# Optimization experiments

Measured on AMD Instinct MI355X. Metric: run time of the kernel, lower is better.

## Reference

```python
import jax, jax.numpy as jnp
import numpy as np


def _sparsify24(w):
    """2:4 structured sparsity: per contiguous group of 4 along the last dim,
    keep the 2 largest-magnitude entries, zero the other 2 (soft_threshold24)."""
    m, n = w.shape
    g = w.reshape(m, n // 4, 4)
    a = jnp.abs(g)
    # 2nd-largest magnitude in each group = index 2 of ascending sort of 4
    thresh = jnp.sort(a, axis=-1)[..., 2:3]
    mask = a >= thresh
    return (g * mask).reshape(m, n)


def setup_inputs() -> dict:
    key = jax.random.key(0)
    k1, k2, k3 = jax.random.split(key, 3)
    B, S, DIN, DOUT = 4, 4096, 1024, 1024
    x = jax.random.normal(k1, (B, S, DIN), dtype=jnp.float32)
    weight = jax.random.normal(k2, (DIN, DOUT), dtype=jnp.float32) * 0.02
    bias = jax.random.normal(k3, (DOUT,), dtype=jnp.float32) * 0.02
    sparse_scale = jnp.ones((1,), dtype=jnp.float32)
    return {"x": x, "weight": weight, "bias": bias, "sparse_scale": sparse_scale}


def reference(x, weight, bias, sparse_scale):
    # get_sparse_weight: cast weight to fp16, apply 2:4 sparsity, multiply by
    # learnable fp32 scale (promotes to fp32 as in torch half*float).
    w_sparse = _sparsify24(weight.astype(jnp.float16)).astype(jnp.float32) * sparse_scale
    # fake_fp8_mm: both operands cast to fp16, accumulate/output in fp32.
    a = x.reshape(-1, x.shape[-1]).astype(jnp.float16)          # [B*S, DIN]
    b = w_sparse.astype(jnp.float16)                             # [DIN, DOUT]
    out = jnp.matmul(a, b, preferred_element_type=jnp.float32)   # [B*S, DOUT] fp32
    out = out.reshape(*x.shape[:-1], -1) + bias
    return out
```

## Files before the change

### kernel.cpp

```cpp
#include <hip/hip_runtime.h>
#include <hip/hip_fp16.h>
#include <stdint.h>

#define M_TOT 16384
#define N_TOT 1024
#define K_TOT 1024

typedef _Float16 f16x8 __attribute__((ext_vector_type(8)));
typedef float f32x4 __attribute__((ext_vector_type(4)));
typedef unsigned short ushort4v __attribute__((ext_vector_type(4)));

__device__ inline void gl2lds16(const void* g, void* l) {
    __builtin_amdgcn_global_load_lds(
        (const __attribute__((address_space(1))) void*)(uintptr_t)(g),
        (__attribute__((address_space(3))) void*)(uint32_t)(uintptr_t)(l),
        16, 0, 0);
}

__global__ void __launch_bounds__(256) prep_and_cast(const float* __restrict__ X,
                                                     const float* __restrict__ W,
                                                     const float* __restrict__ scale_p,
                                                     _Float16* __restrict__ Xh,
                                                     _Float16* __restrict__ wT) {
    const int tid = threadIdx.x;
    if (blockIdx.x < 256) {
        __shared__ _Float16 sT[64 * 68 + 4];
        const float scale = scale_p[0];
        const int k0 = (blockIdx.x & 15) * 64;
        const int n0 = (blockIdx.x >> 4) * 64;
        const int r = tid >> 4;
        const int c4 = (tid & 15) * 4;
#pragma unroll
        for (int p = 0; p < 4; ++p) {
            const int k = p * 16 + r;
            float4 w4 = *(const float4*)&W[(size_t)(k0 + k) * N_TOT + n0 + c4];
            _Float16 h0 = (_Float16)w4.x, h1 = (_Float16)w4.y, h2 = (_Float16)w4.z, h3 = (_Float16)w4.w;
            float a0 = fabsf((float)h0), a1 = fabsf((float)h1), a2 = fabsf((float)h2), a3 = fabsf((float)h3);
            float lo01 = fminf(a0, a1), hi01 = fmaxf(a0, a1);
            float lo23 = fminf(a2, a3), hi23 = fmaxf(a2, a3);
            float s2 = fmaxf(fminf(hi01, hi23), fmaxf(lo01, lo23));
            sT[(c4 + 0) * 68 + k] = (_Float16)(((a0 >= s2) ? (float)h0 : 0.0f) * scale);
            sT[(c4 + 1) * 68 + k] = (_Float16)(((a1 >= s2) ? (float)h1 : 0.0f) * scale);
            sT[(c4 + 2) * 68 + k] = (_Float16)(((a2 >= s2) ? (float)h2 : 0.0f) * scale);
            sT[(c4 + 3) * 68 + k] = (_Float16)(((a3 >= s2) ? (float)h3 : 0.0f) * scale);
        }
        __syncthreads();
#pragma unroll
        for (int p = 0; p < 4; ++p) {
            const int n = p * 16 + r;
            ushort4v v = *(const ushort4v*)&sT[n * 68 + c4];
            *(ushort4v*)&wT[(size_t)(n0 + n) * K_TOT + k0 + c4] = v;
        }
    } else {
        size_t i = ((size_t)(blockIdx.x - 256) * 256 + tid) * 8;
        float4 x0 = *(const float4*)&X[i];
        float4 x1 = *(const float4*)&X[i + 4];
        f16x8 h;
        h[0] = (_Float16)x0.x; h[1] = (_Float16)x0.y; h[2] = (_Float16)x0.z; h[3] = (_Float16)x0.w;
        h[4] = (_Float16)x1.x; h[5] = (_Float16)x1.y; h[6] = (_Float16)x1.z; h[7] = (_Float16)x1.w;
        *(f16x8*)&Xh[i] = h;
    }
}

__global__ void __launch_bounds__(512, 2) gemm_bt(const _Float16* __restrict__ A,
                                                  const _Float16* __restrict__ Bt,
                                                  const float* __restrict__ bias,
                                                  float* __restrict__ C) {
    __shared__ __align__(16) _Float16 sA[2][2][256 * 32];
    __shared__ __align__(16) _Float16 sB[2][2][256 * 32];

    const int tid = threadIdx.x;
    const int id = blockIdx.x;
    const int by = id & 63;
    const int bx = id >> 6;
    const int wave = tid >> 6;
    const int lane = tid & 63;
    const int wm = wave >> 2;
    const int wn = wave & 3;
    const int quad = lane >> 4;
    const int l16 = lane & 15;

    const int row0 = tid >> 2;
    const int s4 = tid & 3;
    const int g = s4 ^ ((row0 >> 1) & 3);
    const _Float16* gA = A + (size_t)(by * 256 + row0) * K_TOT + g * 8;
    const _Float16* gB = Bt + (size_t)(bx * 256 + row0) * K_TOT + g * 8;
    const int dst0 = row0 * 32 + s4 * 8;

    const int rdoff = l16 * 64 + ((quad ^ ((l16 >> 1) & 3)) << 4);

    f32x4 acc[8][4];
#pragma unroll
    for (int i = 0; i < 8; ++i)
#pragma unroll
        for (int j = 0; j < 4; ++j)
            acc[i][j] = (f32x4){0.f, 0.f, 0.f, 0.f};
    f16x8 fa[4], fb[4];

#define STAGE_A(b, kt, kh) do {                                            \
        const _Float16* s_ = gA + (kt) * 64 + (kh) * 32;                   \
        gl2lds16(s_, &sA[b][kh][dst0]);                                    \
        gl2lds16(s_ + (size_t)128 * K_TOT, &sA[b][kh][dst0 + 128 * 32]);   \
    } while (0)
#define STAGE_B(b, kt, kh) do {                                            \
        const _Float16* s_ = gB + (kt) * 64 + (kh) * 32;                   \
        gl2lds16(s_, &sB[b][kh][dst0]);                                    \
        gl2lds16(s_ + (size_t)128 * K_TOT, &sB[b][kh][dst0 + 128 * 32]);   \
    } while (0)
#define FENCE asm volatile("" ::: "memory")
#define WAIT8 asm volatile("s_waitcnt vmcnt(8)" ::: "memory")
#define BAR do { FENCE; __builtin_amdgcn_s_barrier(); FENCE; } while (0)

#define PHASE(b, ks, qm, LOADB, STAGE_STMT) do {                                   \
        {                                                                          \
            const char* bA_ = (const char*)&sA[b][ks][0] + rdoff + wm * 8192 + (qm) * 4096; \
            fa[0] = *(const f16x8*)(bA_);                                          \
            fa[1] = *(const f16x8*)(bA_ + 1024);                                   \
            fa[2] = *(const f16x8*)(bA_ + 2048);                                   \
            fa[3] = *(const f16x8*)(bA_ + 3072);                                   \
            if (LOADB) {                                                           \
                const char* bB_ = (const char*)&sB[b][ks][0] + rdoff + wn * 4096;  \
                fb[0] = *(const f16x8*)(bB_);                                      \
                fb[1] = *(const f16x8*)(bB_ + 1024);                               \
                fb[2] = *(const f16x8*)(bB_ + 2048);                               \
                fb[3] = *(const f16x8*)(bB_ + 3072);                               \
            }                                                                      \
        }                                                                          \
        STAGE_STMT;                                                                \
        BAR;                                                                       \
        __builtin_amdgcn_s_setprio(1);                                             \
        _Pragma("unroll")                                                          \
        for (int ii = 0; ii < 4; ++ii) {                                           \
            _Pragma("unroll")                                                      \
            for (int j = 0; j < 4; ++j)                                            \
                acc[(qm) * 4 + ii][j] = __builtin_amdgcn_mfma_f32_16x16x32_f16(    \
                    fa[ii], fb[j], acc[(qm) * 4 + ii][j], 0, 0, 0);                \
        }                                                                          \
        __builtin_amdgcn_s_setprio(0);                                             \
    } while (0)

    STAGE_A(0, 0, 0); STAGE_B(0, 0, 0);
    STAGE_A(0, 0, 1); STAGE_B(0, 0, 1);
    STAGE_A(1, 1, 0); STAGE_B(1, 1, 0);
    WAIT8;
    BAR;

    for (int it = 0; it < 8; ++it) {
        const int t1 = (2 * it + 1) & 15;
        const int t2 = (2 * it + 2) & 15;
        const int t3 = (2 * it + 3) & 15;
        PHASE(0, 0, 0, 1, STAGE_A(1, t1, 1));        BAR;
        PHASE(0, 0, 1, 0, STAGE_B(1, t1, 1)); WAIT8; BAR;
        PHASE(0, 1, 0, 1, STAGE_A(0, t2, 0));        BAR;
        PHASE(0, 1, 1, 0, STAGE_B(0, t2, 0)); WAIT8; BAR;
        PHASE(1, 0, 0, 1, STAGE_A(0, t2, 1));        BAR;
        PHASE(1, 0, 1, 0, STAGE_B(0, t2, 1)); WAIT8; BAR;
        PHASE(1, 1, 0, 1, STAGE_A(1, t3, 0));        BAR;
        PHASE(1, 1, 1, 0, STAGE_B(1, t3, 0)); WAIT8; BAR;
    }

#pragma unroll
    for (int j = 0; j < 4; ++j) {
        const int col = bx * 256 + wn * 64 + j * 16 + l16;
        const float bj = bias[col];
#pragma unroll
        for (int mi = 0; mi < 8; ++mi) {
            const int row0o = by * 256 + wm * 128 + mi * 16 + quad * 4;
#pragma unroll
            for (int r = 0; r < 4; ++r) {
                C[(size_t)(row0o + r) * N_TOT + col] = acc[mi][j][r] + bj;
            }
        }
    }

#undef PHASE
#undef BAR
#undef WAIT8
#undef FENCE
#undef STAGE_B
#undef STAGE_A
}

extern "C" void kernel_launch(void* const* d_in, const int* in_sizes, int n_in,
                              void* d_out, int out_size, void* d_ws, size_t ws_size,
                              hipStream_t stream) {
    const float* x      = (const float*)d_in[0];
    const float* weight = (const float*)d_in[1];
    const float* bias   = (const float*)d_in[2];
    const float* sscale = (const float*)d_in[3];
    float* out = (float*)d_out;

    _Float16* wT = (_Float16*)d_ws;
    _Float16* xh = (_Float16*)((char*)d_ws + (size_t)2 * 1024 * 1024);

    prep_and_cast<<<256 + (M_TOT * K_TOT / 8) / 256, 256, 0, stream>>>(x, weight, sscale, xh, wT);
    gemm_bt<<<256, 512, 0, stream>>>(xh, wT, bias, out);
}
```

Measured before the change: 152.6 us.

## Replace double-buffered half-tile pipeline with triple-buffered single-barrier K loop

Restructures the GEMM main loop from a double-buffered scheme to a three-stage ring of 32-wide K tiles. Each tile stages A and B together, and each phase needs one wait-and-barrier instead of two barriers. Each phase now loads all eight A fragments and four B fragments and issues 32 MFMAs, which cuts synchronisation overhead and gives loads more lead time. The cost is more vector registers for fragments and a three-buffer LDS footprint, along with waitcnt accounting that depends on an exact count of outstanding loads.

Measured after the change: 152.0 us. No clear change (-0.4%).

```diff
diff --git a/kernel.cpp b/kernel.cpp
--- a/kernel.cpp
+++ b/kernel.cpp
@@ -66,8 +66,8 @@
                                                   const _Float16* __restrict__ Bt,
                                                   const float* __restrict__ bias,
                                                   float* __restrict__ C) {
-    __shared__ __align__(16) _Float16 sA[2][2][256 * 32];
-    __shared__ __align__(16) _Float16 sB[2][2][256 * 32];
+    __shared__ __align__(16) _Float16 sA[3][256 * 32];
+    __shared__ __align__(16) _Float16 sB[3][256 * 32];
 
     const int tid = threadIdx.x;
     const int id = blockIdx.x;
@@ -95,69 +95,55 @@
 #pragma unroll
         for (int j = 0; j < 4; ++j)
             acc[i][j] = (f32x4){0.f, 0.f, 0.f, 0.f};
-    f16x8 fa[4], fb[4];
+    f16x8 fa[8], fb[4];
 
-#define STAGE_A(b, kt, kh) do {                                            \
-        const _Float16* s_ = gA + (kt) * 64 + (kh) * 32;                   \
-        gl2lds16(s_, &sA[b][kh][dst0]);                                    \
-        gl2lds16(s_ + (size_t)128 * K_TOT, &sA[b][kh][dst0 + 128 * 32]);   \
-    } while (0)
-#define STAGE_B(b, kt, kh) do {                                            \
-        const _Float16* s_ = gB + (kt) * 64 + (kh) * 32;                   \
-        gl2lds16(s_, &sB[b][kh][dst0]);                                    \
-        gl2lds16(s_ + (size_t)128 * K_TOT, &sB[b][kh][dst0 + 128 * 32]);   \
+#define STAGE(t, b) do {                                                   \
+        const _Float16* sa_ = gA + (size_t)(t) * 32;                       \
+        gl2lds16(sa_, &sA[b][dst0]);                                       \
+        gl2lds16(sa_ + (size_t)128 * K_TOT, &sA[b][dst0 + 128 * 32]);      \
+        const _Float16* sb_ = gB + (size_t)(t) * 32;                       \
+        gl2lds16(sb_, &sB[b][dst0]);                                       \
+        gl2lds16(sb_ + (size_t)128 * K_TOT, &sB[b][dst0 + 128 * 32]);      \
     } while (0)
 #define FENCE asm volatile("" ::: "memory")
-#define WAIT8 asm volatile("s_waitcnt vmcnt(8)" ::: "memory")
-#define BAR do { FENCE; __builtin_amdgcn_s_barrier(); FENCE; } while (0)
 
-#define PHASE(b, ks, qm, LOADB, STAGE_STMT) do {                                   \
+#define PH(b, t2, b2, DO_STAGE, WLAST) do {                                        \
+        if (WLAST) asm volatile("s_waitcnt vmcnt(0)" ::: "memory");                \
+        else       asm volatile("s_waitcnt vmcnt(4)" ::: "memory");                \
+        __builtin_amdgcn_sched_barrier(0);                                         \
+        __builtin_amdgcn_s_barrier();                                              \
+        FENCE;                                                                     \
+        if (DO_STAGE) STAGE(t2, b2);                                               \
         {                                                                          \
-            const char* bA_ = (const char*)&sA[b][ks][0] + rdoff + wm * 8192 + (qm) * 4096; \
-            fa[0] = *(const f16x8*)(bA_);                                          \
-            fa[1] = *(const f16x8*)(bA_ + 1024);                                   \
-            fa[2] = *(const f16x8*)(bA_ + 2048);                                   \
-            fa[3] = *(const f16x8*)(bA_ + 3072);                                   \
-            if (LOADB) {                                                           \
-                const char* bB_ = (const char*)&sB[b][ks][0] + rdoff + wn * 4096;  \
-                fb[0] = *(const f16x8*)(bB_);                                      \
-                fb[1] = *(const f16x8*)(bB_ + 1024);                               \
-                fb[2] = *(const f16x8*)(bB_ + 2048);                               \
-                fb[3] = *(const f16x8*)(bB_ + 3072);                               \
-            }                                                                      \
+            const char* bA_ = (const char*)&sA[b][0] + rdoff + wm * 8192;          \
+            const char* bB_ = (const char*)&sB[b][0] + rdoff + wn * 4096;          \
+            _Pragma("unroll")                                                      \
+            for (int j = 0; j < 4; ++j) fb[j] = *(const f16x8*)(bB_ + j * 1024);   \
+            _Pragma("unroll")                                                      \
+            for (int i = 0; i < 8; ++i) fa[i] = *(const f16x8*)(bA_ + i * 1024);   \
         }                                                                          \
-        STAGE_STMT;                                                                \
-        BAR;                                                                       \
         __builtin_amdgcn_s_setprio(1);                                             \
         _Pragma("unroll")                                                          \
-        for (int ii = 0; ii < 4; ++ii) {                                           \
+        for (int i = 0; i < 8; ++i) {                                              \
             _Pragma("unroll")                                                      \
             for (int j = 0; j < 4; ++j)                                            \
-                acc[(qm) * 4 + ii][j] = __builtin_amdgcn_mfma_f32_16x16x32_f16(    \
-                    fa[ii], fb[j], acc[(qm) * 4 + ii][j], 0, 0, 0);                \
+                acc[i][j] = __builtin_amdgcn_mfma_f32_16x16x32_f16(                \
+                    fa[i], fb[j], acc[i][j], 0, 0, 0);                             \
         }                                                                          \
         __builtin_amdgcn_s_setprio(0);                                             \
     } while (0)
 
-    STAGE_A(0, 0, 0); STAGE_B(0, 0, 0);
-    STAGE_A(0, 0, 1); STAGE_B(0, 0, 1);
-    STAGE_A(1, 1, 0); STAGE_B(1, 1, 0);
-    WAIT8;
-    BAR;
+    STAGE(0, 0);
+    STAGE(1, 1);
 
-    for (int it = 0; it < 8; ++it) {
-        const int t1 = (2 * it + 1) & 15;
-        const int t2 = (2 * it + 2) & 15;
-        const int t3 = (2 * it + 3) & 15;
-        PHASE(0, 0, 0, 1, STAGE_A(1, t1, 1));        BAR;
-        PHASE(0, 0, 1, 0, STAGE_B(1, t1, 1)); WAIT8; BAR;
-        PHASE(0, 1, 0, 1, STAGE_A(0, t2, 0));        BAR;
-        PHASE(0, 1, 1, 0, STAGE_B(0, t2, 0)); WAIT8; BAR;
-        PHASE(1, 0, 0, 1, STAGE_A(0, t2, 1));        BAR;
-        PHASE(1, 0, 1, 0, STAGE_B(0, t2, 1)); WAIT8; BAR;
-        PHASE(1, 1, 0, 1, STAGE_A(1, t3, 0));        BAR;
-        PHASE(1, 1, 1, 0, STAGE_B(1, t3, 0)); WAIT8; BAR;
+    for (int it = 0; it < 10; ++it) {
+        const int t = 3 * it;
+        PH(0, t + 2, 2, 1, 0);
+        PH(1, t + 3, 0, 1, 0);
+        PH(2, t + 4, 1, 1, 0);
     }
+    PH(0, 0, 0, 0, 0);
+    PH(1, 0, 0, 0, 1);
 
 #pragma unroll
     for (int j = 0; j < 4; ++j) {
@@ -173,12 +159,9 @@
         }
     }
 
-#undef PHASE
-#undef BAR
-#undef WAIT8
+#undef PH
 #undef FENCE
-#undef STAGE_B
-#undef STAGE_A
+#undef STAGE
 }
 
 extern "C" void kernel_launch(void* const* d_in, const int* in_sizes, int n_in,
```
